# Kernel tuning notes

Hardware: AMD Instinct MI355X
Metric: run time of the kernel (lower is better)

Reference implementation:

```python
import jax, jax.numpy as jnp
import numpy as np
import math


def setup_inputs() -> dict:
    key = jax.random.key(0)
    k1, k2, k3 = jax.random.split(key, 3)
    b, h, w = 4, 64, 64
    hw = h * w
    gp_dim = 64
    sim_matrix = jax.random.normal(k1, (b, hw, hw), dtype=jnp.float32)
    conv_w = jax.random.normal(k2, (gp_dim, 2), dtype=jnp.float32)
    conv_b = jax.random.normal(k3, (gp_dim,), dtype=jnp.float32)
    return {"sim_matrix": sim_matrix, "conv_w": conv_w, "conv_b": conv_b,
            "b": b, "h": h, "w": w}


def _pos_enc(conv_w, conv_b, b, h, w):
    # normalized grid coords in (-1, 1), channel 0 = x (width), channel 1 = y (height)
    ys = jnp.linspace(-1.0 + 1.0 / h, 1.0 - 1.0 / h, h, dtype=jnp.float32)
    xs = jnp.linspace(-1.0 + 1.0 / w, 1.0 - 1.0 / w, w, dtype=jnp.float32)
    gy, gx = jnp.meshgrid(ys, xs, indexing="ij")          # [h, w] each
    coords = jnp.stack([gx, gy], axis=0)                   # [2, h, w]
    # 1x1 conv == per-pixel linear: [d,2] @ [2,h,w] + bias
    proj = jnp.einsum("dc,chw->dhw", conv_w, coords) + conv_b[:, None, None]
    f = jnp.cos(8.0 * math.pi * proj)                       # fourier basis, [d, h, w]
    return jnp.broadcast_to(f[None], (b,) + f.shape)        # [b, d, h, w]


def reference(sim_matrix, conv_w, conv_b, b, h, w):
    d = conv_w.shape[0]
    f = _pos_enc(conv_w, conv_b, b, h, w)                   # [b, d, h, w]
    f = f.reshape(b, d, h * w).transpose(0, 2, 1)           # [b, hw, d]
    conf = jax.nn.softmax(sim_matrix, axis=2)               # [b, hw, hw]
    gp = jnp.einsum("bnm,bmd->bnd", conf, f)                # [b, hw, d]
    return gp.transpose(0, 2, 1).reshape(b, d, h, w)        # [b, d, h, w]
```

## Files before the change

### kernel.cpp

```cpp
#include <hip/hip_runtime.h>


typedef _Float16 f16;
typedef f16 f16x8 __attribute__((ext_vector_type(8)));
typedef float f32x4 __attribute__((ext_vector_type(4)));

static constexpr int HW = 4096;
static constexpr int ND = 64;
static constexpr int KW = 8;
static constexpr int KM = HW / KW;

__global__ __launch_bounds__(256) void posenc_f16(
    const float* __restrict__ cw, const float* __restrict__ cb,
    f16* __restrict__ ft)
{
    int g = blockIdx.x * 256 + threadIdx.x;
    int d = g >> 12;
    int m = g & 4095;
    int i = m >> 6;
    int j = m & 63;
    float gx = (float)(2 * j - 63) * (1.0f / 64.0f);
    float gy = (float)(2 * i - 63) * (1.0f / 64.0f);
    float proj = cw[2 * d] * gx + cw[2 * d + 1] * gy + cb[d];
    float v = cosf(25.132741228718345f * proj);
    ft[(size_t)d * HW + m] = (f16)v;
}

__global__ __launch_bounds__(512) void gp_main(
    const float* __restrict__ sim, const f16* __restrict__ ft,
    float* __restrict__ out)
{
    const int bb   = blockIdx.x >> 6;
    const int ng   = blockIdx.x & 63;
    const int wv   = threadIdx.x >> 6;
    const int lane = threadIdx.x & 63;
    const int c    = lane & 15;
    const int q    = lane >> 4;
    const int n0   = ng * 64;

    const float* sbase = sim + (size_t)bb * HW * HW + (size_t)(n0 + c) * HW
                             + wv * KM + q * 8;
    const f16*   fbase = ft + (size_t)c * HW + wv * KM + q * 8;

    f32x4 acc[4][4];
    #pragma unroll
    for (int t = 0; t < 4; t++)
        #pragma unroll
        for (int u = 0; u < 4; u++)
            acc[t][u] = (f32x4){0.f, 0.f, 0.f, 0.f};
    float psum[4] = {0.f, 0.f, 0.f, 0.f};

    for (int m0 = 0; m0 < KM; m0 += 32) {
        f16x8 bfr[4];
        #pragma unroll
        for (int u = 0; u < 4; u++)
            bfr[u] = *(const f16x8*)(fbase + (size_t)u * 16 * HW + m0);

        #pragma unroll
        for (int t = 0; t < 4; t++) {
            const float* sp = sbase + (size_t)t * 16 * HW + m0;
            f32x4 s0 = *(const f32x4*)sp;
            f32x4 s1 = *(const f32x4*)(sp + 4);

            float p0 = __expf(s0[0]);
            float p1 = __expf(s0[1]);
            float p2 = __expf(s0[2]);
            float p3 = __expf(s0[3]);
            float p4 = __expf(s1[0]);
            float p5 = __expf(s1[1]);
            float p6 = __expf(s1[2]);
            float p7 = __expf(s1[3]);
            psum[t] += ((p0 + p1) + (p2 + p3)) + ((p4 + p5) + (p6 + p7));

            f16x8 a;
            a[0] = (f16)p0; a[1] = (f16)p1; a[2] = (f16)p2; a[3] = (f16)p3;
            a[4] = (f16)p4; a[5] = (f16)p5; a[6] = (f16)p6; a[7] = (f16)p7;

            #pragma unroll
            for (int u = 0; u < 4; u++)
                acc[t][u] = __builtin_amdgcn_mfma_f32_16x16x32_f16(
                    a, bfr[u], acc[t][u], 0, 0, 0);
        }
    }

    __shared__ f32x4 red[KW][8][64];
    __shared__ float rsum[KW][4][64];

    #pragma unroll
    for (int t = 0; t < 4; t++)
        rsum[wv][t][lane] = psum[t];

    #pragma unroll
    for (int ph = 0; ph < 2; ph++) {
        const int tb = ph * 2;
        if (ph)
            __syncthreads();
        #pragma unroll
        for (int t = 0; t < 2; t++)
            #pragma unroll
            for (int u = 0; u < 4; u++)
                red[wv][t * 4 + u][lane] = acc[tb + t][u];
        __syncthreads();

        const int t = tb + (wv >> 2);
        const int u = wv & 3;
        f32x4 A = red[0][wv][lane];
        #pragma unroll
        for (int s = 1; s < KW; s++)
            A += red[s][wv][lane];
        float ps = 0.f;
        #pragma unroll
        for (int s = 0; s < KW; s++)
            ps += rsum[s][t][lane];
        ps += __shfl_xor(ps, 16, 64);
        ps += __shfl_xor(ps, 32, 64);
        float r0 = 1.0f / __shfl(ps, q * 4 + 0, 64);
        float r1 = 1.0f / __shfl(ps, q * 4 + 1, 64);
        float r2 = 1.0f / __shfl(ps, q * 4 + 2, 64);
        float r3 = 1.0f / __shfl(ps, q * 4 + 3, 64);

        f32x4 v;
        v[0] = A[0] * r0; v[1] = A[1] * r1; v[2] = A[2] * r2; v[3] = A[3] * r3;
        *(f32x4*)(out + (size_t)bb * ND * HW + (size_t)(u * 16 + c) * HW
                  + n0 + t * 16 + q * 4) = v;
    }
}

extern "C" void kernel_launch(void* const* d_in, const int* in_sizes, int n_in,
                              void* d_out, int out_size, void* d_ws, size_t ws_size,
                              hipStream_t stream) {
    (void)in_sizes; (void)n_in; (void)out_size; (void)ws_size;
    const float* sim = (const float*)d_in[0];
    const float* cw  = (const float*)d_in[1];
    const float* cb  = (const float*)d_in[2];
    float* out = (float*)d_out;
    f16* ft = (f16*)d_ws;

    posenc_f16<<<(ND * HW) / 256, 256, 0, stream>>>(cw, cb, ft);
    gp_main<<<256, 512, 0, stream>>>(sim, ft, out);
}
```

Before: 371.1 us.

## Halve rows per block, double grid, software-prefetch sim with nontemporal loads

Each block now handles 32 query rows instead of 64, doubling the grid to 512 blocks to fill more compute units and cut per-thread accumulator registers (launch bounds request 4 blocks per CU). The sim stream is double-buffered in registers, issuing the next chunk's loads before the current chunk's exp and MFMA work, and uses nontemporal loads to avoid polluting cache. The reduction collapses to a single phase. In exchange, the f16 positional features are re-read by twice as many blocks.

```diff
diff --git a/kernel.cpp b/kernel.cpp
--- a/kernel.cpp
+++ b/kernel.cpp
@@ -26,104 +26,122 @@
     ft[(size_t)d * HW + m] = (f16)v;
 }
 
-__global__ __launch_bounds__(512) void gp_main(
+
+__device__ __forceinline__ void gp_step_t(
+    const f32x4 s0, const f32x4 s1, const f16x8 bfr[4],
+    f32x4 acc[4], float& ps)
+{
+    float p0 = __expf(s0[0]); float p1 = __expf(s0[1]);
+    float p2 = __expf(s0[2]); float p3 = __expf(s0[3]);
+    float p4 = __expf(s1[0]); float p5 = __expf(s1[1]);
+    float p6 = __expf(s1[2]); float p7 = __expf(s1[3]);
+    ps += ((p0 + p1) + (p2 + p3)) + ((p4 + p5) + (p6 + p7));
+    f16x8 a;
+    a[0] = (f16)p0; a[1] = (f16)p1; a[2] = (f16)p2; a[3] = (f16)p3;
+    a[4] = (f16)p4; a[5] = (f16)p5; a[6] = (f16)p6; a[7] = (f16)p7;
+    #pragma unroll
+    for (int u = 0; u < 4; u++)
+        acc[u] = __builtin_amdgcn_mfma_f32_16x16x32_f16(
+            a, bfr[u], acc[u], 0, 0, 0);
+}
+
+#define NTLOAD(p) __builtin_nontemporal_load((const f32x4*)(p))
+
+__global__ __launch_bounds__(512, 4) void gp_main(
     const float* __restrict__ sim, const f16* __restrict__ ft,
     float* __restrict__ out)
 {
-    const int bb   = blockIdx.x >> 6;
-    const int ng   = blockIdx.x & 63;
+    const int bb   = blockIdx.x >> 7;
+    const int ng   = blockIdx.x & 127;
     const int wv   = threadIdx.x >> 6;
     const int lane = threadIdx.x & 63;
     const int c    = lane & 15;
     const int q    = lane >> 4;
-    const int n0   = ng * 64;
+    const int n0   = ng * 32;
 
     const float* sbase = sim + (size_t)bb * HW * HW + (size_t)(n0 + c) * HW
                              + wv * KM + q * 8;
     const f16*   fbase = ft + (size_t)c * HW + wv * KM + q * 8;
 
-    f32x4 acc[4][4];
+    f32x4 acc[2][4];
     #pragma unroll
-    for (int t = 0; t < 4; t++)
+    for (int t = 0; t < 2; t++)
         #pragma unroll
         for (int u = 0; u < 4; u++)
             acc[t][u] = (f32x4){0.f, 0.f, 0.f, 0.f};
-    float psum[4] = {0.f, 0.f, 0.f, 0.f};
+    float psum[2] = {0.f, 0.f};
 
-    for (int m0 = 0; m0 < KM; m0 += 32) {
-        f16x8 bfr[4];
-        #pragma unroll
-        for (int u = 0; u < 4; u++)
-            bfr[u] = *(const f16x8*)(fbase + (size_t)u * 16 * HW + m0);
+    f32x4 sa0 = NTLOAD(sbase);
+    f32x4 sa1 = NTLOAD(sbase + 4);
+    f32x4 sa2 = NTLOAD(sbase + (size_t)16 * HW);
+    f32x4 sa3 = NTLOAD(sbase + (size_t)16 * HW + 4);
 
-        #pragma unroll
-        for (int t = 0; t < 4; t++) {
-            const float* sp = sbase + (size_t)t * 16 * HW + m0;
-            f32x4 s0 = *(const f32x4*)sp;
-            f32x4 s1 = *(const f32x4*)(sp + 4);
+    for (int m0 = 0; m0 < KM; m0 += 64) {
+        f32x4 sb0 = NTLOAD(sbase + m0 + 32);
+        f32x4 sb1 = NTLOAD(sbase + m0 + 36);
+        f32x4 sb2 = NTLOAD(sbase + (size_t)16 * HW + m0 + 32);
+        f32x4 sb3 = NTLOAD(sbase + (size_t)16 * HW + m0 + 36);
 
-            float p0 = __expf(s0[0]);
-            float p1 = __expf(s0[1]);
-            float p2 = __expf(s0[2]);
-            float p3 = __expf(s0[3]);
-            float p4 = __expf(s1[0]);
-            float p5 = __expf(s1[1]);
-            float p6 = __expf(s1[2]);
-            float p7 = __expf(s1[3]);
-            psum[t] += ((p0 + p1) + (p2 + p3)) + ((p4 + p5) + (p6 + p7));
-
-            f16x8 a;
-            a[0] = (f16)p0; a[1] = (f16)p1; a[2] = (f16)p2; a[3] = (f16)p3;
-            a[4] = (f16)p4; a[5] = (f16)p5; a[6] = (f16)p6; a[7] = (f16)p7;
-
+        {
+            f16x8 bfr[4];
             #pragma unroll
             for (int u = 0; u < 4; u++)
-                acc[t][u] = __builtin_amdgcn_mfma_f32_16x16x32_f16(
-                    a, bfr[u], acc[t][u], 0, 0, 0);
+                bfr[u] = *(const f16x8*)(fbase + (size_t)u * 16 * HW + m0);
+            gp_step_t(sa0, sa1, bfr, acc[0], psum[0]);
+            gp_step_t(sa2, sa3, bfr, acc[1], psum[1]);
+        }
+
+        if (m0 + 64 < KM) {
+            sa0 = NTLOAD(sbase + m0 + 64);
+            sa1 = NTLOAD(sbase + m0 + 68);
+            sa2 = NTLOAD(sbase + (size_t)16 * HW + m0 + 64);
+            sa3 = NTLOAD(sbase + (size_t)16 * HW + m0 + 68);
+        }
+
+        {
+            f16x8 bfr[4];
+            #pragma unroll
+            for (int u = 0; u < 4; u++)
+                bfr[u] = *(const f16x8*)(fbase + (size_t)u * 16 * HW + m0 + 32);
+            gp_step_t(sb0, sb1, bfr, acc[0], psum[0]);
+            gp_step_t(sb2, sb3, bfr, acc[1], psum[1]);
         }
     }
 
     __shared__ f32x4 red[KW][8][64];
-    __shared__ float rsum[KW][4][64];
+    __shared__ float rsum[KW][2][64];
 
     #pragma unroll
-    for (int t = 0; t < 4; t++)
+    for (int t = 0; t < 2; t++)
         rsum[wv][t][lane] = psum[t];
+    #pragma unroll
+    for (int t = 0; t < 2; t++)
+        #pragma unroll
+        for (int u = 0; u < 4; u++)
+            red[wv][t * 4 + u][lane] = acc[t][u];
+    __syncthreads();
 
+    const int t = wv >> 2;
+    const int u = wv & 3;
+    f32x4 A = red[0][wv][lane];
     #pragma unroll
-    for (int ph = 0; ph < 2; ph++) {
-        const int tb = ph * 2;
-        if (ph)
-            __syncthreads();
-        #pragma unroll
-        for (int t = 0; t < 2; t++)
-            #pragma unroll
-            for (int u = 0; u < 4; u++)
-                red[wv][t * 4 + u][lane] = acc[tb + t][u];
-        __syncthreads();
+    for (int s = 1; s < KW; s++)
+        A += red[s][wv][lane];
+    float ps = 0.f;
+    #pragma unroll
+    for (int s = 0; s < KW; s++)
+        ps += rsum[s][t][lane];
+    ps += __shfl_xor(ps, 16, 64);
+    ps += __shfl_xor(ps, 32, 64);
+    float r0 = 1.0f / __shfl(ps, q * 4 + 0, 64);
+    float r1 = 1.0f / __shfl(ps, q * 4 + 1, 64);
+    float r2 = 1.0f / __shfl(ps, q * 4 + 2, 64);
+    float r3 = 1.0f / __shfl(ps, q * 4 + 3, 64);
 
-        const int t = tb + (wv >> 2);
-        const int u = wv & 3;
-        f32x4 A = red[0][wv][lane];
-        #pragma unroll
-        for (int s = 1; s < KW; s++)
-            A += red[s][wv][lane];
-        float ps = 0.f;
-        #pragma unroll
-        for (int s = 0; s < KW; s++)
-            ps += rsum[s][t][lane];
-        ps += __shfl_xor(ps, 16, 64);
-        ps += __shfl_xor(ps, 32, 64);
-        float r0 = 1.0f / __shfl(ps, q * 4 + 0, 64);
-        float r1 = 1.0f / __shfl(ps, q * 4 + 1, 64);
-        float r2 = 1.0f / __shfl(ps, q * 4 + 2, 64);
-        float r3 = 1.0f / __shfl(ps, q * 4 + 3, 64);
-
-        f32x4 v;
-        v[0] = A[0] * r0; v[1] = A[1] * r1; v[2] = A[2] * r2; v[3] = A[3] * r3;
-        *(f32x4*)(out + (size_t)bb * ND * HW + (size_t)(u * 16 + c) * HW
-                  + n0 + t * 16 + q * 4) = v;
-    }
+    f32x4 v;
+    v[0] = A[0] * r0; v[1] = A[1] * r1; v[2] = A[2] * r2; v[3] = A[3] * r3;
+    *(f32x4*)(out + (size_t)bb * ND * HW + (size_t)(u * 16 + c) * HW
+              + n0 + t * 16 + q * 4) = v;
 }
 
 extern "C" void kernel_launch(void* const* d_in, const int* in_sizes, int n_in,
@@ -137,5 +155,5 @@
     f16* ft = (f16*)d_ws;
 
     posenc_f16<<<(ND * HW) / 256, 256, 0, stream>>>(cw, cb, ft);
-    gp_main<<<256, 512, 0, stream>>>(sim, ft, out);
+    gp_main<<<512, 512, 0, stream>>>(sim, ft, out);
 }
```

After: 376.3 us. About the same (+1.4%).
